# Optimization experiments

Measured on AMD Instinct MI355X. Metric: run time of the kernel, lower is better.

Reference implementation:

```python
import jax, jax.numpy as jnp
import numpy as np

N = 100000      # nodes
E = 1600000     # edges
F_IN = 128      # in_features
H = 128         # num_hiddens
L = 4           # num_layers
G = 256         # graphs in batch
ENC = 256       # encoder out
DEC = 128       # decoder hidden
EPS = 1e-5


def setup_inputs() -> dict:
    key = jax.random.key(0)
    ks = jax.random.split(key, 12)
    x = jax.random.normal(ks[0], (N, F_IN), dtype=jnp.float32)
    edge_index = jax.random.randint(ks[1], (2, E), 0, N, dtype=jnp.int32)
    batch = jnp.sort(jax.random.randint(ks[2], (N,), 0, G, dtype=jnp.int32))
    s_h = 1.0 / np.sqrt(H)
    conv_W = jax.random.normal(ks[3], (L, H, H), dtype=jnp.float32) * s_h  # layer0 in=F_IN==H
    conv_b = jax.random.normal(ks[4], (L, H), dtype=jnp.float32) * 0.01
    bn_gamma = jnp.ones((L, H), dtype=jnp.float32)
    bn_beta = jnp.zeros((L, H), dtype=jnp.float32)
    enc_W = jax.random.normal(ks[5], (L * H, ENC), dtype=jnp.float32) / np.sqrt(L * H)
    enc_b = jax.random.normal(ks[6], (ENC,), dtype=jnp.float32) * 0.01
    dec_W1 = jax.random.normal(ks[7], (ENC, DEC), dtype=jnp.float32) / np.sqrt(ENC)
    dec_b1 = jax.random.normal(ks[8], (DEC,), dtype=jnp.float32) * 0.01
    dec_W2 = jax.random.normal(ks[9], (DEC, 1), dtype=jnp.float32) / np.sqrt(DEC)
    dec_b2 = jax.random.normal(ks[10], (1,), dtype=jnp.float32) * 0.01
    return {"x": x, "edge_index": edge_index, "batch": batch,
            "conv_W": conv_W, "conv_b": conv_b,
            "bn_gamma": bn_gamma, "bn_beta": bn_beta,
            "enc_W": enc_W, "enc_b": enc_b,
            "dec_W1": dec_W1, "dec_b1": dec_b1,
            "dec_W2": dec_W2, "dec_b2": dec_b2}


def _gcn_layer(h, W, b, src, dst, dinv):
    # GCNConv: add self-loops, symmetric D^{-1/2} (A+I) D^{-1/2} (h @ W) + b
    hw = h @ W                                        # [N, H]
    norm = dinv[src] * dinv[dst]                      # [E]
    msg = norm[:, None] * hw[src]                     # [E, H] gathered messages
    agg = jax.ops.segment_sum(msg, dst, num_segments=N)
    agg = agg + (dinv * dinv)[:, None] * hw           # self-loop term
    return agg + b


def _bn_relu(h, gamma, beta):
    mu = jnp.mean(h, axis=0)
    var = jnp.var(h, axis=0)
    return jax.nn.relu((h - mu) * jax.lax.rsqrt(var + EPS) * gamma + beta)


def reference(x, edge_index, batch, conv_W, conv_b, bn_gamma, bn_beta,
              enc_W, enc_b, dec_W1, dec_b1, dec_W2, dec_b2):
    src, dst = edge_index[0], edge_index[1]
    # degree with self-loops (in-degree at dst, +1 per node)
    deg = jax.ops.segment_sum(jnp.ones((E,), jnp.float32), dst, num_segments=N) + 1.0
    dinv = jax.lax.rsqrt(deg)
    h = x
    layer_out = []
    for l in range(L):
        h = _gcn_layer(h, conv_W[l], conv_b[l], src, dst, dinv)
        h = _bn_relu(h, bn_gamma[l], bn_beta[l])
        layer_out.append(h)
    hk = jnp.concatenate(layer_out, axis=-1)          # JK 'cat' -> [N, L*H]
    enc = jax.nn.relu(hk @ enc_W + enc_b)             # [N, ENC]
    # scatter_mean over batch -> [G, ENC]
    summed = jax.ops.segment_sum(enc, batch, num_segments=G)
    counts = jax.ops.segment_sum(jnp.ones((N,), jnp.float32), batch, num_segments=G)
    pooled = summed / jnp.maximum(counts, 1.0)[:, None]
    hidden = jax.nn.relu(pooled @ dec_W1 + dec_b1)
    out = hidden @ dec_W2 + dec_b2                    # [G, 1]
    return jnp.squeeze(out, axis=1)                   # num_classes == 1
```

## Files before the change

kernel.cpp:

```cpp
#include <hip/hip_runtime.h>
#include <hip/hip_bf16.h>

#define N_NODES 100000
#define NPAD    100096
#define N_EDGES 1600000
#define HDIM 128
#define NLAYERS 4
#define NGRAPH 256
#define ENCDIM 256
#define EPS_BN 1e-5f
#define BN_BLOCKS 512

typedef __attribute__((ext_vector_type(8))) short bf16x8;
typedef __attribute__((ext_vector_type(4))) float f32x4;

__device__ __forceinline__ unsigned short f2bf(float v) {
    unsigned int u = __float_as_uint(v);
    u += 0x7FFFu + ((u >> 16) & 1u);
    return (unsigned short)(u >> 16);
}
__device__ __forceinline__ float bf2f(unsigned int lo16) {
    return __uint_as_float(lo16 << 16);
}

__global__ void k_count(const int* __restrict__ dst, int* __restrict__ cnt) {
    int e = blockIdx.x * 256 + threadIdx.x;
    if (e < N_EDGES) atomicAdd(&cnt[dst[e]], 1);
}

__global__ void k_dinv(const int* __restrict__ cnt, float* __restrict__ dinv) {
    int n = blockIdx.x * 256 + threadIdx.x;
    if (n < N_NODES) dinv[n] = rsqrtf((float)cnt[n] + 1.0f);
}

__global__ void k_scan_block(const int* __restrict__ cnt, int* __restrict__ excl,
                             int* __restrict__ bsums) {
    __shared__ int s[256];
    int t = threadIdx.x;
    int i = blockIdx.x * 256 + t;
    int v = (i < N_NODES) ? cnt[i] : 0;
    s[t] = v;
    __syncthreads();
    for (int off = 1; off < 256; off <<= 1) {
        int x = 0;
        if (t >= off) x = s[t - off];
        __syncthreads();
        if (t >= off) s[t] += x;
        __syncthreads();
    }
    if (i < N_NODES) excl[i] = s[t] - v;
    if (t == 255) bsums[blockIdx.x] = s[255];
}

__global__ void k_scan_sums(int* __restrict__ bsums, int nb) {
    __shared__ int s[512];
    int t = threadIdx.x;
    int v = (t < nb) ? bsums[t] : 0;
    s[t] = v;
    __syncthreads();
    for (int off = 1; off < 512; off <<= 1) {
        int x = 0;
        if (t >= off) x = s[t - off];
        __syncthreads();
        if (t >= off) s[t] += x;
        __syncthreads();
    }
    if (t < nb) bsums[t] = s[t] - v;
}

__global__ void k_scan_add(int* __restrict__ excl, const int* __restrict__ bsums,
                           int* __restrict__ cursor) {
    int i = blockIdx.x * 256 + threadIdx.x;
    if (i < N_NODES) {
        int v = excl[i] + bsums[blockIdx.x];
        excl[i] = v;
        cursor[i] = v;
    }
}

__global__ void k_scatter(const int* __restrict__ src, const int* __restrict__ dst,
                          const float* __restrict__ dinv, int* __restrict__ cursor,
                          int2* __restrict__ csr_ew) {
    int e = blockIdx.x * 256 + threadIdx.x;
    if (e < N_EDGES) {
        int d = dst[e];
        int s = src[e];
        int p = atomicAdd(&cursor[d], 1);
        int2 v;
        v.x = s;
        v.y = __float_as_int(dinv[s] * dinv[d]);
        csr_ew[p] = v;
    }
}

__global__ void k_gbounds(const int* __restrict__ batch, int* __restrict__ gstart,
                          int* __restrict__ gcnt) {
    __shared__ int s[257];
    int g = threadIdx.x;
    int lo = 0, hi = N_NODES;
    while (lo < hi) {
        int mid = (lo + hi) >> 1;
        if (batch[mid] < g) lo = mid + 1; else hi = mid;
    }
    s[g] = lo;
    if (g == 255) s[256] = N_NODES;
    __syncthreads();
    gstart[g] = s[g];
    gcnt[g] = s[g + 1] - s[g];
}

__global__ void k_wfrag(const float* __restrict__ W, int ldw, int ntiles,
                        unsigned short* __restrict__ Fh, unsigned short* __restrict__ Fl) {
    int t = blockIdx.x * 256 + threadIdx.x;
    if (t >= ntiles * 256) return;
    int lane = t & 63, ks = (t >> 6) & 3, nt = t >> 8;
    int r16 = lane & 15, kq = lane >> 4;
    unsigned short h[8], l[8];
#pragma unroll
    for (int j = 0; j < 8; j++) {
        float w = W[(size_t)(ks * 32 + kq * 8 + j) * ldw + nt * 16 + r16];
        unsigned short hh = f2bf(w);
        h[j] = hh;
        l[j] = f2bf(w - bf2f(hh));
    }
    ((ushort4*)(Fh + (size_t)t * 8))[0] = make_ushort4(h[0], h[1], h[2], h[3]);
    ((ushort4*)(Fh + (size_t)t * 8))[1] = make_ushort4(h[4], h[5], h[6], h[7]);
    ((ushort4*)(Fl + (size_t)t * 8))[0] = make_ushort4(l[0], l[1], l[2], l[3]);
    ((ushort4*)(Fl + (size_t)t * 8))[1] = make_ushort4(l[4], l[5], l[6], l[7]);
}

__device__ __forceinline__ void load_a_frag(const float* __restrict__ A, size_t row,
                                            bool ok, int kq, int ks,
                                            bf16x8& hv_out, bf16x8& lv_out) {
    float4 v0 = make_float4(0.f, 0.f, 0.f, 0.f);
    float4 v1 = make_float4(0.f, 0.f, 0.f, 0.f);
    if (ok) {
        const float* pa = A + row * 128 + kq * 8 + ks * 32;
        v0 = *(const float4*)pa;
        v1 = *(const float4*)(pa + 4);
    }
    float vv[8] = {v0.x, v0.y, v0.z, v0.w, v1.x, v1.y, v1.z, v1.w};
    bf16x8 hv, lv;
#pragma unroll
    for (int j = 0; j < 8; j++) {
        unsigned short hh = f2bf(vv[j]);
        hv[j] = (short)hh;
        lv[j] = (short)f2bf(vv[j] - bf2f(hh));
    }
    hv_out = hv;
    lv_out = lv;
}

__global__ __launch_bounds__(256) void k_mfma_f32(const float* __restrict__ A,
                                                  const unsigned short* __restrict__ Fh,
                                                  const unsigned short* __restrict__ Fl,
                                                  unsigned short* __restrict__ Cb) {
    int lane = threadIdx.x & 63;
    int wid = threadIdx.x >> 6;
    int r16 = lane & 15, kq = lane >> 4;
    size_t mrow0 = (size_t)blockIdx.x * 128 + wid * 32;

    bf16x8 ah[2][4], al[2][4];
#pragma unroll
    for (int mt = 0; mt < 2; mt++) {
        size_t row = mrow0 + mt * 16 + r16;
        bool ok = row < N_NODES;
#pragma unroll
        for (int ks = 0; ks < 4; ks++)
            load_a_frag(A, row, ok, kq, ks, ah[mt][ks], al[mt][ks]);
    }

    f32x4 acc[2][8];
#pragma unroll
    for (int mt = 0; mt < 2; mt++)
#pragma unroll
        for (int nt = 0; nt < 8; nt++) acc[mt][nt] = (f32x4){0.f, 0.f, 0.f, 0.f};

#pragma unroll
    for (int nt = 0; nt < 8; nt++) {
        const unsigned short* pbh = Fh + ((size_t)nt * 4 * 64 + lane) * 8;
        const unsigned short* pbl = Fl + ((size_t)nt * 4 * 64 + lane) * 8;
        bf16x8 bh[4], bl[4];
#pragma unroll
        for (int ks = 0; ks < 4; ks++) {
            bh[ks] = *reinterpret_cast<const bf16x8*>(pbh + ks * 512);
            bl[ks] = *reinterpret_cast<const bf16x8*>(pbl + ks * 512);
        }
#pragma unroll
        for (int mt = 0; mt < 2; mt++)
#pragma unroll
            for (int ks = 0; ks < 4; ks++) {
                acc[mt][nt] = __builtin_amdgcn_mfma_f32_16x16x32_bf16(ah[mt][ks], bl[ks],
                                                                     acc[mt][nt], 0, 0, 0);
                acc[mt][nt] = __builtin_amdgcn_mfma_f32_16x16x32_bf16(al[mt][ks], bh[ks],
                                                                     acc[mt][nt], 0, 0, 0);
                acc[mt][nt] = __builtin_amdgcn_mfma_f32_16x16x32_bf16(ah[mt][ks], bh[ks],
                                                                     acc[mt][nt], 0, 0, 0);
            }
    }

#pragma unroll
    for (int mt = 0; mt < 2; mt++)
#pragma unroll
        for (int nt = 0; nt < 8; nt++)
#pragma unroll
            for (int r = 0; r < 4; r++) {
                size_t row = mrow0 + mt * 16 + kq * 4 + r;
                Cb[row * 128 + nt * 16 + r16] = f2bf(acc[mt][nt][r]);
            }
}

__global__ __launch_bounds__(256) void k_mfma_bf(const unsigned short* __restrict__ A,
                                                 const unsigned short* __restrict__ Fh,
                                                 const unsigned short* __restrict__ Fl,
                                                 unsigned short* __restrict__ Cb) {
    int lane = threadIdx.x & 63;
    int wid = threadIdx.x >> 6;
    int r16 = lane & 15, kq = lane >> 4;
    size_t mrow0 = (size_t)blockIdx.x * 128 + wid * 32;

    bf16x8 ah[2][4];
#pragma unroll
    for (int mt = 0; mt < 2; mt++) {
        size_t row = mrow0 + mt * 16 + r16;
        bool ok = row < N_NODES;
#pragma unroll
        for (int ks = 0; ks < 4; ks++) {
            if (ok)
                ah[mt][ks] = *reinterpret_cast<const bf16x8*>(
                    A + row * 128 + ks * 32 + kq * 8);
            else
                ah[mt][ks] = (bf16x8){0, 0, 0, 0, 0, 0, 0, 0};
        }
    }

    f32x4 acc[2][8];
#pragma unroll
    for (int mt = 0; mt < 2; mt++)
#pragma unroll
        for (int nt = 0; nt < 8; nt++) acc[mt][nt] = (f32x4){0.f, 0.f, 0.f, 0.f};

#pragma unroll
    for (int nt = 0; nt < 8; nt++) {
        const unsigned short* pbh = Fh + ((size_t)nt * 4 * 64 + lane) * 8;
        const unsigned short* pbl = Fl + ((size_t)nt * 4 * 64 + lane) * 8;
        bf16x8 bh[4], bl[4];
#pragma unroll
        for (int ks = 0; ks < 4; ks++) {
            bh[ks] = *reinterpret_cast<const bf16x8*>(pbh + ks * 512);
            bl[ks] = *reinterpret_cast<const bf16x8*>(pbl + ks * 512);
        }
#pragma unroll
        for (int mt = 0; mt < 2; mt++)
#pragma unroll
            for (int ks = 0; ks < 4; ks++) {
                acc[mt][nt] = __builtin_amdgcn_mfma_f32_16x16x32_bf16(ah[mt][ks], bl[ks],
                                                                     acc[mt][nt], 0, 0, 0);
                acc[mt][nt] = __builtin_amdgcn_mfma_f32_16x16x32_bf16(ah[mt][ks], bh[ks],
                                                                     acc[mt][nt], 0, 0, 0);
            }
    }

#pragma unroll
    for (int mt = 0; mt < 2; mt++)
#pragma unroll
        for (int nt = 0; nt < 8; nt++)
#pragma unroll
            for (int r = 0; r < 4; r++) {
                size_t row = mrow0 + mt * 16 + kq * 4 + r;
                Cb[row * 128 + nt * 16 + r16] = f2bf(acc[mt][nt][r]);
            }
}

__global__ __launch_bounds__(256) void k_enc_pool(
    const unsigned short* __restrict__ Ub0, const unsigned short* __restrict__ Ub1,
    const unsigned short* __restrict__ Ub2, const unsigned short* __restrict__ Ub3,
    const unsigned short* __restrict__ Fh, const unsigned short* __restrict__ Fl,
    const float* __restrict__ encB, const int* __restrict__ batch,
    float* __restrict__ psum) {
    int lane = threadIdx.x & 63;
    int wid = threadIdx.x >> 6;
    int r16 = lane & 15, kq = lane >> 4;
    size_t brow0 = (size_t)blockIdx.x * 128;
    size_t mrow0 = brow0 + wid * 32;
    int colOff = blockIdx.y * 128;
    int ntBase = blockIdx.y * 8;

    __shared__ int batch_lds[128];
    if (threadIdx.x < 128) {
        size_t row = brow0 + threadIdx.x;
        batch_lds[threadIdx.x] = (row < N_NODES) ? batch[row] : -1;
    }
    __syncthreads();

    f32x4 acc[2][8];
#pragma unroll
    for (int mt = 0; mt < 2; mt++)
#pragma unroll
        for (int nt = 0; nt < 8; nt++) acc[mt][nt] = (f32x4){0.f, 0.f, 0.f, 0.f};

    const unsigned short* Ubs[4] = {Ub0, Ub1, Ub2, Ub3};
#pragma unroll 1
    for (int l = 0; l < 4; l++) {
        const unsigned short* Ub = Ubs[l];
        bf16x8 ah[2][4];
#pragma unroll
        for (int mt = 0; mt < 2; mt++) {
            size_t row = mrow0 + mt * 16 + r16;
            bool ok = row < N_NODES;
#pragma unroll
            for (int ks = 0; ks < 4; ks++) {
                if (ok)
                    ah[mt][ks] = *reinterpret_cast<const bf16x8*>(
                        Ub + row * 128 + ks * 32 + kq * 8);
                else
                    ah[mt][ks] = (bf16x8){0, 0, 0, 0, 0, 0, 0, 0};
            }
        }
        const unsigned short* Fhl = Fh + (size_t)l * 32768;
        const unsigned short* Fll = Fl + (size_t)l * 32768;
#pragma unroll
        for (int nt = 0; nt < 8; nt++) {
            const unsigned short* pbh = Fhl + ((size_t)(ntBase + nt) * 4 * 64 + lane) * 8;
            const unsigned short* pbl = Fll + ((size_t)(ntBase + nt) * 4 * 64 + lane) * 8;
            bf16x8 bh[4], bl[4];
#pragma unroll
            for (int ks = 0; ks < 4; ks++) {
                bh[ks] = *reinterpret_cast<const bf16x8*>(pbh + ks * 512);
                bl[ks] = *reinterpret_cast<const bf16x8*>(pbl + ks * 512);
            }
#pragma unroll
            for (int mt = 0; mt < 2; mt++)
#pragma unroll
                for (int ks = 0; ks < 4; ks++) {
                    acc[mt][nt] = __builtin_amdgcn_mfma_f32_16x16x32_bf16(
                        ah[mt][ks], bl[ks], acc[mt][nt], 0, 0, 0);
                    acc[mt][nt] = __builtin_amdgcn_mfma_f32_16x16x32_bf16(
                        ah[mt][ks], bh[ks], acc[mt][nt], 0, 0, 0);
                }
        }
    }

    float bias[8];
#pragma unroll
    for (int nt = 0; nt < 8; nt++) bias[nt] = encB[colOff + nt * 16 + r16];
#pragma unroll
    for (int mt = 0; mt < 2; mt++)
#pragma unroll
        for (int r = 0; r < 4; r++) {
            bool valid = batch_lds[wid * 32 + mt * 16 + kq * 4 + r] >= 0;
#pragma unroll
            for (int nt = 0; nt < 8; nt++)
                acc[mt][nt][r] = valid ? fmaxf(acc[mt][nt][r] + bias[nt], 0.f) : 0.f;
        }

    int lastIdx = (int)((N_NODES - 1 - brow0) < 127 ? (N_NODES - 1 - brow0) : 127);
    int g0 = batch_lds[0];
    int g1 = batch_lds[lastIdx];
    __shared__ float sred[4][128];
    for (int g = g0; g <= g1; ++g) {
        float s[8];
#pragma unroll
        for (int nt = 0; nt < 8; nt++) s[nt] = 0.f;
#pragma unroll
        for (int mt = 0; mt < 2; mt++)
#pragma unroll
            for (int r = 0; r < 4; r++) {
                bool m = batch_lds[wid * 32 + mt * 16 + kq * 4 + r] == g;
                if (m) {
#pragma unroll
                    for (int nt = 0; nt < 8; nt++) s[nt] += acc[mt][nt][r];
                }
            }
#pragma unroll
        for (int nt = 0; nt < 8; nt++) {
            s[nt] += __shfl_xor(s[nt], 16);
            s[nt] += __shfl_xor(s[nt], 32);
        }
        if (lane < 16) {
#pragma unroll
            for (int nt = 0; nt < 8; nt++) sred[wid][nt * 16 + r16] = s[nt];
        }
        __syncthreads();
        if (threadIdx.x < 128) {
            float tot = sred[0][threadIdx.x] + sred[1][threadIdx.x] +
                        sred[2][threadIdx.x] + sred[3][threadIdx.x];
            atomicAdd(&psum[(size_t)g * ENCDIM + colOff + threadIdx.x], tot);
        }
        __syncthreads();
    }
}

__global__ __launch_bounds__(256) void k_agg(const unsigned short* __restrict__ hwb,
                                             const int* __restrict__ rs,
                                             const int* __restrict__ cnt,
                                             const int2* __restrict__ csr_ew,
                                             const float* __restrict__ dinv,
                                             const float4* __restrict__ bias4,
                                             unsigned short* __restrict__ Ub) {
    int n = blockIdx.x * 8 + (threadIdx.x >> 5);
    int lane = threadIdx.x & 31;
    if (n >= N_NODES) return;
    float d = dinv[n];
    float dd = d * d;
    ushort4 sb = *(const ushort4*)(hwb + (size_t)n * 128 + lane * 4);
    float4 b = bias4[lane];
    float4 acc;
    acc.x = fmaf(dd, bf2f(sb.x), b.x);
    acc.y = fmaf(dd, bf2f(sb.y), b.y);
    acc.z = fmaf(dd, bf2f(sb.z), b.z);
    acc.w = fmaf(dd, bf2f(sb.w), b.w);
    int s0 = rs[n];
    int c = cnt[n];
    int e = 0;
    for (; e + 8 <= c; e += 8) {
        int2 ee[8];
        ushort4 vv[8];
#pragma unroll
        for (int u = 0; u < 8; u++) ee[u] = csr_ew[s0 + e + u];
#pragma unroll
        for (int u = 0; u < 8; u++)
            vv[u] = *(const ushort4*)(hwb + (size_t)ee[u].x * 128 + lane * 4);
#pragma unroll
        for (int u = 0; u < 8; u++) {
            float w = __int_as_float(ee[u].y);
            acc.x = fmaf(w, bf2f(vv[u].x), acc.x);
            acc.y = fmaf(w, bf2f(vv[u].y), acc.y);
            acc.z = fmaf(w, bf2f(vv[u].z), acc.z);
            acc.w = fmaf(w, bf2f(vv[u].w), acc.w);
        }
    }
    for (; e < c; e++) {
        int2 ee = csr_ew[s0 + e];
        ushort4 v = *(const ushort4*)(hwb + (size_t)ee.x * 128 + lane * 4);
        float w = __int_as_float(ee.y);
        acc.x = fmaf(w, bf2f(v.x), acc.x);
        acc.y = fmaf(w, bf2f(v.y), acc.y);
        acc.z = fmaf(w, bf2f(v.z), acc.z);
        acc.w = fmaf(w, bf2f(v.w), acc.w);
    }
    ushort4 bv;
    bv.x = f2bf(acc.x);
    bv.y = f2bf(acc.y);
    bv.z = f2bf(acc.z);
    bv.w = f2bf(acc.w);
    *(ushort4*)(Ub + (size_t)n * 128 + lane * 4) = bv;
}

__global__ __launch_bounds__(256) void k_bn_stats(const uint4* __restrict__ Ub4,
                                                  float* __restrict__ part_sum,
                                                  float* __restrict__ part_sq) {
    int c = threadIdx.x & 15;
    int y = threadIdx.x >> 4;
    float s[8], q[8];
#pragma unroll
    for (int j = 0; j < 8; j++) { s[j] = 0.f; q[j] = 0.f; }
    for (size_t n = (size_t)blockIdx.x * 16 + y; n < N_NODES;
         n += (size_t)gridDim.x * 16) {
        uint4 v = Ub4[n * 16 + c];
        float a[8];
        a[0] = bf2f(v.x & 0xffffu); a[1] = bf2f(v.x >> 16);
        a[2] = bf2f(v.y & 0xffffu); a[3] = bf2f(v.y >> 16);
        a[4] = bf2f(v.z & 0xffffu); a[5] = bf2f(v.z >> 16);
        a[6] = bf2f(v.w & 0xffffu); a[7] = bf2f(v.w >> 16);
#pragma unroll
        for (int j = 0; j < 8; j++) {
            s[j] += a[j];
            q[j] = fmaf(a[j], a[j], q[j]);
        }
    }
    __shared__ float ls[256][9], lq[256][9];
#pragma unroll
    for (int j = 0; j < 8; j++) {
        ls[threadIdx.x][j] = s[j];
        lq[threadIdx.x][j] = q[j];
    }
    __syncthreads();
    if (y == 0) {
#pragma unroll
        for (int yy = 1; yy < 16; yy++)
#pragma unroll
            for (int j = 0; j < 8; j++) {
                s[j] += ls[yy * 16 + c][j];
                q[j] += lq[yy * 16 + c][j];
            }
#pragma unroll
        for (int j = 0; j < 8; j++) {
            part_sum[(size_t)blockIdx.x * 128 + c * 8 + j] = s[j];
            part_sq[(size_t)blockIdx.x * 128 + c * 8 + j] = q[j];
        }
    }
}

__global__ void k_bn_finalize(const float* __restrict__ part_sum,
                              const float* __restrict__ part_sq,
                              const float* __restrict__ gamma,
                              const float* __restrict__ beta,
                              float* __restrict__ scale, float* __restrict__ shift) {
    int f = threadIdx.x;
    float s = 0.f, q = 0.f;
#pragma unroll 4
    for (int b = 0; b < BN_BLOCKS; b++) {
        s += part_sum[(size_t)b * 128 + f];
        q += part_sq[(size_t)b * 128 + f];
    }
    float mu = s * (1.0f / N_NODES);
    float var = q * (1.0f / N_NODES) - mu * mu;
    float sc = rsqrtf(var + EPS_BN) * gamma[f];
    scale[f] = sc;
    shift[f] = beta[f] - mu * sc;
}

__global__ __launch_bounds__(256) void k_bnapply(uint4* __restrict__ Ub4,
                                                 const float* __restrict__ scale,
                                                 const float* __restrict__ shift) {
    size_t i = (size_t)blockIdx.x * 256 + threadIdx.x;
    int f0 = (int)(i & 15) * 8;
    float4 sc0 = *(const float4*)&scale[f0];
    float4 sc1 = *(const float4*)&scale[f0 + 4];
    float4 sh0 = *(const float4*)&shift[f0];
    float4 sh1 = *(const float4*)&shift[f0 + 4];
    uint4 v = Ub4[i];
    float a0 = fmaxf(fmaf(bf2f(v.x & 0xffffu), sc0.x, sh0.x), 0.f);
    float a1 = fmaxf(fmaf(bf2f(v.x >> 16), sc0.y, sh0.y), 0.f);
    float a2 = fmaxf(fmaf(bf2f(v.y & 0xffffu), sc0.z, sh0.z), 0.f);
    float a3 = fmaxf(fmaf(bf2f(v.y >> 16), sc0.w, sh0.w), 0.f);
    float a4 = fmaxf(fmaf(bf2f(v.z & 0xffffu), sc1.x, sh1.x), 0.f);
    float a5 = fmaxf(fmaf(bf2f(v.z >> 16), sc1.y, sh1.y), 0.f);
    float a6 = fmaxf(fmaf(bf2f(v.w & 0xffffu), sc1.z, sh1.z), 0.f);
    float a7 = fmaxf(fmaf(bf2f(v.w >> 16), sc1.w, sh1.w), 0.f);
    uint4 o;
    o.x = (unsigned int)f2bf(a0) | ((unsigned int)f2bf(a1) << 16);
    o.y = (unsigned int)f2bf(a2) | ((unsigned int)f2bf(a3) << 16);
    o.z = (unsigned int)f2bf(a4) | ((unsigned int)f2bf(a5) << 16);
    o.w = (unsigned int)f2bf(a6) | ((unsigned int)f2bf(a7) << 16);
    Ub4[i] = o;
}

__global__ __launch_bounds__(128) void k_dec(const float* __restrict__ psum,
                                             const int* __restrict__ gcnt,
                                             const float* __restrict__ W1,
                                             const float* __restrict__ b1,
                                             const float* __restrict__ W2,
                                             const float* __restrict__ b2,
                                             float* __restrict__ out) {
    int g = blockIdx.x;
    int j = threadIdx.x;
    float inv = 1.0f / fmaxf((float)gcnt[g], 1.0f);
    const float* p = &psum[g * ENCDIM];
    float acc = b1[j];
    for (int k = 0; k < ENCDIM; k++) acc = fmaf(p[k] * inv, W1[k * 128 + j], acc);
    float h = fmaxf(acc, 0.f) * W2[j];
    for (int off = 32; off; off >>= 1) h += __shfl_down(h, off);
    __shared__ float red[2];
    if ((j & 63) == 0) red[j >> 6] = h;
    __syncthreads();
    if (j == 0) out[g] = red[0] + red[1] + b2[0];
}

extern "C" void kernel_launch(void* const* d_in, const int* in_sizes, int n_in,
                              void* d_out, int out_size, void* d_ws, size_t ws_size,
                              hipStream_t stream) {
    const float* x = (const float*)d_in[0];
    const int* ei = (const int*)d_in[1];
    const int* src = ei;
    const int* dst = ei + N_EDGES;
    const int* batch = (const int*)d_in[2];
    const float* convW = (const float*)d_in[3];
    const float* convB = (const float*)d_in[4];
    const float* gamma = (const float*)d_in[5];
    const float* beta = (const float*)d_in[6];
    const float* encW = (const float*)d_in[7];
    const float* encB = (const float*)d_in[8];
    const float* dW1 = (const float*)d_in[9];
    const float* db1 = (const float*)d_in[10];
    const float* dW2 = (const float*)d_in[11];
    const float* db2 = (const float*)d_in[12];
    float* out = (float*)d_out;

    char* w = (char*)d_ws;
    auto alloc = [&](size_t bytes) {
        char* p = w;
        w += (bytes + 255) & ~(size_t)255;
        return p;
    };
    int* cnt = (int*)alloc((size_t)N_NODES * 4);
    int* rs = (int*)alloc((size_t)N_NODES * 4);
    int* cursor = (int*)alloc((size_t)N_NODES * 4);
    int* bsums = (int*)alloc(512 * 4);
    float* dinv = (float*)alloc((size_t)N_NODES * 4);
    int2* csr_ew = (int2*)alloc((size_t)N_EDGES * 8);
    unsigned short* B = (unsigned short*)alloc((size_t)NPAD * HDIM * 2);
    unsigned short* Ubf[NLAYERS];
    for (int l = 0; l < NLAYERS; l++)
        Ubf[l] = (unsigned short*)alloc((size_t)NPAD * HDIM * 2);
    unsigned short* convWfh = (unsigned short*)alloc((size_t)NLAYERS * 16384 * 2);
    unsigned short* convWfl = (unsigned short*)alloc((size_t)NLAYERS * 16384 * 2);
    unsigned short* encWfh = (unsigned short*)alloc((size_t)NLAYERS * 32768 * 2);
    unsigned short* encWfl = (unsigned short*)alloc((size_t)NLAYERS * 32768 * 2);
    float* part_sum = (float*)alloc((size_t)BN_BLOCKS * 128 * 4);
    float* part_sq = (float*)alloc((size_t)BN_BLOCKS * 128 * 4);
    float* bnscaleAll = (float*)alloc(NLAYERS * 128 * 4);
    float* bnshiftAll = (float*)alloc(NLAYERS * 128 * 4);
    int* gcnt = (int*)alloc(256 * 4);
    int* gstart = (int*)alloc(256 * 4);
    float* psum = (float*)alloc(256 * 256 * 4);

    hipMemsetAsync(cnt, 0, (size_t)N_NODES * 4, stream);
    hipMemsetAsync(psum, 0, 256 * 256 * 4, stream);

    k_count<<<(N_EDGES + 255) / 256, 256, 0, stream>>>(dst, cnt);
    k_dinv<<<(N_NODES + 255) / 256, 256, 0, stream>>>(cnt, dinv);
    int nb = (N_NODES + 255) / 256;
    k_scan_block<<<nb, 256, 0, stream>>>(cnt, rs, bsums);
    k_scan_sums<<<1, 512, 0, stream>>>(bsums, nb);
    k_scan_add<<<nb, 256, 0, stream>>>(rs, bsums, cursor);
    k_scatter<<<(N_EDGES + 255) / 256, 256, 0, stream>>>(src, dst, dinv, cursor, csr_ew);
    k_gbounds<<<1, 256, 0, stream>>>(batch, gstart, gcnt);

    for (int l = 0; l < NLAYERS; l++) {
        k_wfrag<<<8, 256, 0, stream>>>(convW + (size_t)l * 16384, 128, 8,
                                       convWfh + (size_t)l * 16384,
                                       convWfl + (size_t)l * 16384);
        k_wfrag<<<16, 256, 0, stream>>>(encW + (size_t)l * 128 * 256, 256, 16,
                                        encWfh + (size_t)l * 32768,
                                        encWfl + (size_t)l * 32768);
    }

    for (int l = 0; l < NLAYERS; l++) {
        if (l == 0)
            k_mfma_f32<<<NPAD / 128, 256, 0, stream>>>(
                x, convWfh + (size_t)l * 16384, convWfl + (size_t)l * 16384, B);
        else
            k_mfma_bf<<<NPAD / 128, 256, 0, stream>>>(
                Ubf[l - 1], convWfh + (size_t)l * 16384, convWfl + (size_t)l * 16384, B);
        k_agg<<<N_NODES / 8, 256, 0, stream>>>(B, rs, cnt, csr_ew, dinv,
                                               (const float4*)(convB + l * 128), Ubf[l]);
        k_bn_stats<<<BN_BLOCKS, 256, 0, stream>>>((const uint4*)Ubf[l], part_sum, part_sq);
        k_bn_finalize<<<1, 128, 0, stream>>>(part_sum, part_sq,
                                             gamma + l * 128, beta + l * 128,
                                             bnscaleAll + l * 128, bnshiftAll + l * 128);
        k_bnapply<<<NPAD * 16 / 256, 256, 0, stream>>>((uint4*)Ubf[l],
                                                       bnscaleAll + l * 128,
                                                       bnshiftAll + l * 128);
    }

    k_enc_pool<<<dim3(NPAD / 128, 2), 256, 0, stream>>>(
        Ubf[0], Ubf[1], Ubf[2], Ubf[3], encWfh, encWfl, encB, batch, psum);
    k_dec<<<256, 128, 0, stream>>>(psum, gcnt, dW1, db1, dW2, db2, out);
}
```

Measured before the change: 858.5 us.

## Batch edges per thread in count/scatter and prefetch next-layer A tiles in encoder

The count and scatter kernels now handle four edges per thread, with fewer blocks. Scatter issues all of its loads, weight products and atomics as grouped batches to raise memory-level parallelism. The encoder-pool kernel prefetches the next layer's activation fragments into registers while it runs MFMAs on the current layer, and gets a launch-bounds occupancy hint. BN stats drop to fewer partial blocks, and the finalize loop is unrolled further. The gain in latency hiding is paid for with extra register pressure in the encoder kernel and lower parallelism in the stats pass.

```diff
diff --git a/kernel.cpp b/kernel.cpp
--- a/kernel.cpp
+++ b/kernel.cpp
@@ -9,7 +9,7 @@
 #define NGRAPH 256
 #define ENCDIM 256
 #define EPS_BN 1e-5f
-#define BN_BLOCKS 512
+#define BN_BLOCKS 256
 
 typedef __attribute__((ext_vector_type(8))) short bf16x8;
 typedef __attribute__((ext_vector_type(4))) float f32x4;
@@ -24,8 +24,12 @@
 }
 
 __global__ void k_count(const int* __restrict__ dst, int* __restrict__ cnt) {
-    int e = blockIdx.x * 256 + threadIdx.x;
-    if (e < N_EDGES) atomicAdd(&cnt[dst[e]], 1);
+    int base = blockIdx.x * 1024 + threadIdx.x;
+#pragma unroll
+    for (int u = 0; u < 4; u++) {
+        int e = base + u * 256;
+        if (e < N_EDGES) atomicAdd(&cnt[dst[e]], 1);
+    }
 }
 
 __global__ void k_dinv(const int* __restrict__ cnt, float* __restrict__ dinv) {
@@ -81,16 +85,32 @@
 __global__ void k_scatter(const int* __restrict__ src, const int* __restrict__ dst,
                           const float* __restrict__ dinv, int* __restrict__ cursor,
                           int2* __restrict__ csr_ew) {
-    int e = blockIdx.x * 256 + threadIdx.x;
-    if (e < N_EDGES) {
-        int d = dst[e];
-        int s = src[e];
-        int p = atomicAdd(&cursor[d], 1);
-        int2 v;
-        v.x = s;
-        v.y = __float_as_int(dinv[s] * dinv[d]);
-        csr_ew[p] = v;
-    }
+    int base = blockIdx.x * 1024 + threadIdx.x;
+    int s[4], d[4];
+    bool ok[4];
+#pragma unroll
+    for (int u = 0; u < 4; u++) {
+        int e = base + u * 256;
+        ok[u] = e < N_EDGES;
+        s[u] = ok[u] ? src[e] : 0;
+        d[u] = ok[u] ? dst[e] : 0;
+    }
+    float ww[4];
+#pragma unroll
+    for (int u = 0; u < 4; u++)
+        if (ok[u]) ww[u] = dinv[s[u]] * dinv[d[u]];
+    int p[4];
+#pragma unroll
+    for (int u = 0; u < 4; u++)
+        if (ok[u]) p[u] = atomicAdd(&cursor[d[u]], 1);
+#pragma unroll
+    for (int u = 0; u < 4; u++)
+        if (ok[u]) {
+            int2 v;
+            v.x = s[u];
+            v.y = __float_as_int(ww[u]);
+            csr_ew[p[u]] = v;
+        }
 }
 
 __global__ void k_gbounds(const int* __restrict__ batch, int* __restrict__ gstart,
@@ -272,7 +292,7 @@
             }
 }
 
-__global__ __launch_bounds__(256) void k_enc_pool(
+__global__ __launch_bounds__(256, 4) void k_enc_pool(
     const unsigned short* __restrict__ Ub0, const unsigned short* __restrict__ Ub1,
     const unsigned short* __restrict__ Ub2, const unsigned short* __restrict__ Ub3,
     const unsigned short* __restrict__ Fh, const unsigned short* __restrict__ Fl,
@@ -300,21 +320,32 @@
         for (int nt = 0; nt < 8; nt++) acc[mt][nt] = (f32x4){0.f, 0.f, 0.f, 0.f};
 
     const unsigned short* Ubs[4] = {Ub0, Ub1, Ub2, Ub3};
+    bf16x8 ah[2][4];
+#pragma unroll
+    for (int mt = 0; mt < 2; mt++) {
+        size_t row = mrow0 + mt * 16 + r16;
+        bool ok = row < N_NODES;
+#pragma unroll
+        for (int ks = 0; ks < 4; ks++)
+            ah[mt][ks] = ok ? *reinterpret_cast<const bf16x8*>(
+                                  Ub0 + row * 128 + ks * 32 + kq * 8)
+                            : (bf16x8){0, 0, 0, 0, 0, 0, 0, 0};
+    }
+
 #pragma unroll 1
     for (int l = 0; l < 4; l++) {
-        const unsigned short* Ub = Ubs[l];
-        bf16x8 ah[2][4];
-#pragma unroll
-        for (int mt = 0; mt < 2; mt++) {
-            size_t row = mrow0 + mt * 16 + r16;
-            bool ok = row < N_NODES;
-#pragma unroll
-            for (int ks = 0; ks < 4; ks++) {
-                if (ok)
-                    ah[mt][ks] = *reinterpret_cast<const bf16x8*>(
-                        Ub + row * 128 + ks * 32 + kq * 8);
-                else
-                    ah[mt][ks] = (bf16x8){0, 0, 0, 0, 0, 0, 0, 0};
+        bf16x8 ahn[2][4];
+        if (l < 3) {
+            const unsigned short* Un = Ubs[l + 1];
+#pragma unroll
+            for (int mt = 0; mt < 2; mt++) {
+                size_t row = mrow0 + mt * 16 + r16;
+                bool ok = row < N_NODES;
+#pragma unroll
+                for (int ks = 0; ks < 4; ks++)
+                    ahn[mt][ks] = ok ? *reinterpret_cast<const bf16x8*>(
+                                           Un + row * 128 + ks * 32 + kq * 8)
+                                     : (bf16x8){0, 0, 0, 0, 0, 0, 0, 0};
             }
         }
         const unsigned short* Fhl = Fh + (size_t)l * 32768;
@@ -338,6 +369,12 @@
                     acc[mt][nt] = __builtin_amdgcn_mfma_f32_16x16x32_bf16(
                         ah[mt][ks], bh[ks], acc[mt][nt], 0, 0, 0);
                 }
+        }
+        if (l < 3) {
+#pragma unroll
+            for (int mt = 0; mt < 2; mt++)
+#pragma unroll
+                for (int ks = 0; ks < 4; ks++) ah[mt][ks] = ahn[mt][ks];
         }
     }
 
@@ -499,7 +536,7 @@
                               float* __restrict__ scale, float* __restrict__ shift) {
     int f = threadIdx.x;
     float s = 0.f, q = 0.f;
-#pragma unroll 4
+#pragma unroll 8
     for (int b = 0; b < BN_BLOCKS; b++) {
         s += part_sum[(size_t)b * 128 + f];
         q += part_sq[(size_t)b * 128 + f];
@@ -609,13 +646,14 @@
     hipMemsetAsync(cnt, 0, (size_t)N_NODES * 4, stream);
     hipMemsetAsync(psum, 0, 256 * 256 * 4, stream);
 
-    k_count<<<(N_EDGES + 255) / 256, 256, 0, stream>>>(dst, cnt);
+    k_count<<<(N_EDGES + 1023) / 1024, 256, 0, stream>>>(dst, cnt);
     k_dinv<<<(N_NODES + 255) / 256, 256, 0, stream>>>(cnt, dinv);
     int nb = (N_NODES + 255) / 256;
     k_scan_block<<<nb, 256, 0, stream>>>(cnt, rs, bsums);
     k_scan_sums<<<1, 512, 0, stream>>>(bsums, nb);
     k_scan_add<<<nb, 256, 0, stream>>>(rs, bsums, cursor);
-    k_scatter<<<(N_EDGES + 255) / 256, 256, 0, stream>>>(src, dst, dinv, cursor, csr_ew);
+    k_scatter<<<(N_EDGES + 1023) / 1024, 256, 0, stream>>>(src, dst, dinv, cursor,
+                                                           csr_ew);
     k_gbounds<<<1, 256, 0, stream>>>(batch, gstart, gcnt);
 
     for (int l = 0; l < NLAYERS; l++) {
@@ -636,7 +674,8 @@
                 Ubf[l - 1], convWfh + (size_t)l * 16384, convWfl + (size_t)l * 16384, B);
         k_agg<<<N_NODES / 8, 256, 0, stream>>>(B, rs, cnt, csr_ew, dinv,
                                                (const float4*)(convB + l * 128), Ubf[l]);
-        k_bn_stats<<<BN_BLOCKS, 256, 0, stream>>>((const uint4*)Ubf[l], part_sum, part_sq);
+        k_bn_stats<<<BN_BLOCKS, 256, 0, stream>>>((const uint4*)Ubf[l], part_sum,
+                                                  part_sq);
         k_bn_finalize<<<1, 128, 0, stream>>>(part_sum, part_sq,
                                              gamma + l * 128, beta + l * 128,
                                              bnscaleAll + l * 128, bnshiftAll + l * 128);
```

Result: faster. 831.8 us (-3.1%).
